# Optimization experiments

Hardware: AMD Instinct MI355X
Metric: run time of the kernel (lower is better)

The kernel has to match this reference:

```python
import jax, jax.numpy as jnp
import numpy as np

RES = 64
NU = 0.002
DX = 2.0 * np.pi / RES
DT = 0.001
M1 = 12
M2 = 12
WIDTH = 32


def _central(x, axis, dx):
    # periodic central difference via roll (matches torch.roll semantics)
    return (jnp.roll(x, -1, axis) - jnp.roll(x, 1, axis)) / (2.0 * dx)


def _grad_module(u):
    # TurbulenceRCLN.compute_grad_u: central diff in x,y; j==2 branch is u*0.1 (kept faithfully)
    g0 = _central(u, 2, DX)
    g1 = _central(u, 3, DX)
    g2 = u * 0.1
    return jnp.stack([g0, g1, g2], axis=2)  # (B,3,3,N,N,N) indexed [b,i,j]


def _grad_solver(u):
    # NavierStokesSolver._compute_gradient: true central differences in all 3 dirs
    return jnp.stack([_central(u, 2 + j, DX) for j in range(3)], axis=2)


def _laplacian(u):
    lap = jnp.zeros_like(u)
    for ax in (2, 3, 4):
        lap = lap + (jnp.roll(u, -1, ax) - 2.0 * u + jnp.roll(u, 1, ax)) / (DX * DX)
    return lap


def _div_tau(tau):
    # tau: (B,3,3,N,N,N); div_i = sum_j d tau_ij / dx_j
    return sum(_central(tau[:, :, j], 2 + j, DX) for j in range(3))


def _spectral_conv(x, w1, w2):
    # x: (B,C,N,N); w1/w2: (C,C,M1,M2,2) real/imag
    N = x.shape[-1]
    xft = jnp.fft.rfft2(x)  # (B,C,N,N//2+1) complex
    w1c = w1[..., 0] + 1j * w1[..., 1]
    w2c = w2[..., 0] + 1j * w2[..., 1]
    a = jnp.einsum('bixy,ioxy->boxy', xft[:, :, :M1, :M2], w1c)
    b = jnp.einsum('bixy,ioxy->boxy', xft[:, :, -M1:, :M2], w2c)
    out = jnp.zeros_like(xft).at[:, :, :M1, :M2].set(a).at[:, :, -M1:, :M2].set(b)
    return jnp.fft.irfft2(out, s=(N, N))


def _fno2d(x, fc0_w, fc0_b, spec_w1, spec_w2, conv_w, conv_b, fc1_w, fc1_b, fc2_w, fc2_b):
    h = jnp.einsum('bcxy,cd->bdxy', x, fc0_w) + fc0_b[None, :, None, None]
    for l in range(4):
        s = _spectral_conv(h, spec_w1[l], spec_w2[l])
        w = jnp.einsum('bcxy,co->boxy', h, conv_w[l]) + conv_b[l][None, :, None, None]
        h = s + w
        if l < 3:
            h = jax.nn.gelu(h)
    h = jax.nn.gelu(jnp.einsum('bcxy,cd->bdxy', h, fc1_w) + fc1_b[None, :, None, None])
    return jnp.einsum('bcxy,cd->bdxy', h, fc2_w) + fc2_b[None, :, None, None]


def setup_inputs() -> dict:
    key = jax.random.key(0)
    ks = jax.random.split(key, 8)
    B = 16
    scale = 1.0 / (WIDTH * WIDTH)
    return {
        'velocity': jax.random.normal(ks[0], (B, 3, RES, RES, RES), jnp.float32),
        'fc0_w': jax.random.normal(ks[1], (10, WIDTH), jnp.float32) * 0.1,
        'fc0_b': jnp.zeros((WIDTH,), jnp.float32),
        'spec_w1': jax.random.normal(ks[2], (4, WIDTH, WIDTH, M1, M2, 2), jnp.float32) * scale,
        'spec_w2': jax.random.normal(ks[3], (4, WIDTH, WIDTH, M1, M2, 2), jnp.float32) * scale,
        'conv_w': jax.random.normal(ks[4], (4, WIDTH, WIDTH), jnp.float32) * 0.1,
        'conv_b': jnp.zeros((4, WIDTH), jnp.float32),
        'fc1_w': jax.random.normal(ks[5], (WIDTH, 128), jnp.float32) * 0.1,
        'fc1_b': jnp.zeros((128,), jnp.float32),
        'fc2_w': jax.random.normal(ks[6], (128, 6), jnp.float32) * 0.1,
        'fc2_b': jnp.zeros((6,), jnp.float32),
    }


def reference(velocity, fc0_w, fc0_b, spec_w1, spec_w2, conv_w, conv_b, fc1_w, fc1_b, fc2_w, fc2_b):
    B = velocity.shape[0]
    N = RES
    # --- soft-shell closure input ---
    grad_u = _grad_module(velocity)                                   # (B,3,3,N,N,N)
    S = 0.5 * (grad_u + jnp.swapaxes(grad_u, 1, 2))
    S_mag = jnp.sqrt(2.0 * jnp.sum(S * S, axis=(1, 2), keepdims=True))  # (B,1,1,N,N,N)
    g_slice = grad_u[:, :, :, :, N // 2, :].reshape(B, 9, N, N)        # 9 grad channels at mid-plane
    s_slice = S_mag[:, :, :, :, N // 2, :].reshape(B, 1, N, N)         # 1 strain-mag channel
    closure_in = jnp.concatenate([g_slice, s_slice], axis=1)          # (B,10,N,N)
    tau2d = _fno2d(closure_in, fc0_w, fc0_b, spec_w1, spec_w2, conv_w, conv_b,
                   fc1_w, fc1_b, fc2_w, fc2_b)                         # (B,6,N,N)
    t = jnp.broadcast_to(tau2d[..., None], (B, 6, N, N, N))           # expand along z
    # reconstruct symmetric stress tensor (B,3,3,N,N,N)
    row0 = jnp.stack([t[:, 0], t[:, 3], t[:, 4]], axis=1)
    row1 = jnp.stack([t[:, 3], t[:, 1], t[:, 5]], axis=1)
    row2 = jnp.stack([t[:, 4], t[:, 5], t[:, 2]], axis=1)
    tau_full = jnp.stack([row0, row1, row2], axis=1)
    # --- hard-core NS step ---
    g = _grad_solver(velocity)
    lap = _laplacian(velocity)
    convection = jnp.einsum('bixyz,bijxyz->bjxyz', velocity, g)
    div_tau = _div_tau(tau_full)
    return velocity + DT * (-convection + NU * lap + div_tau)
```

## Files before the change

kernel.cpp:

```cpp
#include <hip/hip_runtime.h>
#include <math.h>

#define NRES 64
#define NXY  4096
#define NVOL 262144
#define BB   16
#define WID  32
#define MM   12
#define R24  24

constexpr double DX_d   = 2.0 * 3.14159265358979323846 / 64.0;
constexpr float  INV2DX = (float)(1.0 / (2.0 * DX_d));
constexpr float  INVDX2 = (float)(1.0 / (DX_d * DX_d));
constexpr float  DT_c   = 0.001f;
constexpr float  NU_c   = 0.002f;

constexpr size_t OFF_FR  = 0;
constexpr size_t OFF_FI  = OFF_FR + (size_t)R24 * NRES;
constexpr size_t OFF_GR  = OFF_FI + (size_t)R24 * NRES;
constexpr size_t OFF_GI  = OFF_GR + (size_t)MM * NRES;
constexpr size_t OFF_CL  = OFF_GI + (size_t)MM * NRES;
constexpr size_t OFF_HA  = OFF_CL + (size_t)BB * 10 * NXY;
constexpr size_t OFF_HB  = OFF_HA + (size_t)BB * WID * NXY;
constexpr size_t OFF_T1R = OFF_HB + (size_t)BB * WID * NXY;
constexpr size_t OFF_T1I = OFF_T1R + (size_t)BB * WID * R24 * NRES;
constexpr size_t OFF_XR  = OFF_T1I + (size_t)BB * WID * R24 * NRES;
constexpr size_t OFF_XI  = OFF_XR + (size_t)BB * WID * R24 * MM;
constexpr size_t OFF_MR  = OFF_XI + (size_t)BB * WID * R24 * MM;
constexpr size_t OFF_MI  = OFF_MR + (size_t)BB * WID * R24 * MM;
constexpr size_t OFF_AR  = OFF_MI + (size_t)BB * WID * R24 * MM;
constexpr size_t OFF_AI  = OFF_AR + (size_t)BB * WID * MM * NRES;
constexpr size_t OFF_H1  = OFF_AI + (size_t)BB * WID * MM * NRES;
constexpr size_t OFF_TAU = OFF_H1 + (size_t)BB * 128 * NXY;
constexpr size_t OFF_FRT = OFF_TAU + (size_t)BB * 6 * NXY;
constexpr size_t OFF_FIT = OFF_FRT + (size_t)NRES * R24;

constexpr size_t OFF_SP  = OFF_H1;
constexpr size_t OFF_W1T = OFF_H1 + (size_t)BB * WID * NXY;
constexpr size_t OFF_CWT = OFF_W1T + 4096;
constexpr size_t OFF_W0T = OFF_CWT + 4096;
constexpr size_t OFF_PT  = OFF_T1R;
constexpr size_t PT_STRIDE = (size_t)BB * 6 * NXY;

__device__ __forceinline__ float gelu_fast(float x) {
    float z = 0.79788456080286535588f * (x + 0.044715f * x * x * x);
    float e = __expf(2.0f * z);
    float t = 1.0f - 2.0f / (e + 1.0f);
    return 0.5f * x * (1.0f + t);
}

__device__ __forceinline__ float2 gelu2(float2 v) {
    return make_float2(gelu_fast(v.x), gelu_fast(v.y));
}

__global__ void k_setup(const float* __restrict__ fc1w, const float* __restrict__ convw,
                        const float* __restrict__ fc0w, float* __restrict__ ws) {
    int idx = blockIdx.x * 256 + threadIdx.x;
    if (idx < R24 * NRES) {
        int r = idx / NRES, x = idx % NRES;
        int kx = (r < MM) ? r : (r + 40);
        double ang = -2.0 * 3.14159265358979323846 * (double)(kx * x) / 64.0;
        float cr = (float)cos(ang), ci = (float)sin(ang);
        ws[OFF_FR + idx] = cr;
        ws[OFF_FI + idx] = ci;
        ws[OFF_FRT + (size_t)x * R24 + r] = cr;
        ws[OFF_FIT + (size_t)x * R24 + r] = ci;
    }
    if (idx < MM * NRES) {
        int ky = idx / NRES, y = idx % NRES;
        double ang = -2.0 * 3.14159265358979323846 * (double)(ky * y) / 64.0;
        ws[OFF_GR + idx] = (float)cos(ang);
        ws[OFF_GI + idx] = (float)sin(ang);
    }
    if (idx < 4096) {
        int c = idx >> 7, e = idx & 127;
        ws[OFF_W1T + (size_t)e * 32 + c] = fc1w[idx];
    } else if (idx < 8192) {
        int j = idx - 4096;
        int l = j >> 10, r = j & 1023;
        int c = r >> 5, o = r & 31;
        ws[OFF_CWT + (size_t)l * 1024 + o * 32 + c] = convw[j];
    } else if (idx < 8512) {
        int j = idx - 8192;
        int c = j >> 5, d = j & 31;
        ws[OFF_W0T + (size_t)d * 10 + c] = fc0w[j];
    }
}

__global__ void k_clfc0(const float* __restrict__ v, const float* __restrict__ w0t,
                        const float* __restrict__ bias, float* __restrict__ h) {
    __shared__ __align__(16) float sw[32 * 12];
    __shared__ float sb[32];
    int tid = threadIdx.x;
    for (int i = tid; i < 320; i += 256) {
        int d = i / 10, c = i % 10;
        sw[d * 12 + c] = w0t[i];
    }
    if (tid < 32) sb[tid] = bias[tid];
    __syncthreads();
    int idx = blockIdx.x * 256 + tid;
    int b = idx >> 10;
    int rr = idx & 1023;
    int x = rr >> 4, z0 = (rr & 15) * 4;
    int xp = (x + 1) & 63, xm = (x - 1) & 63;
    float4 cv[10];
    for (int i = 0; i < 3; i++) {
        const float* vb = v + (((size_t)(b * 3 + i)) << 18);
        float4 u4   = *(const float4*)(vb + (size_t)x  * 4096 + 32 * 64 + z0);
        float4 uxp4 = *(const float4*)(vb + (size_t)xp * 4096 + 32 * 64 + z0);
        float4 uxm4 = *(const float4*)(vb + (size_t)xm * 4096 + 32 * 64 + z0);
        float4 uyp4 = *(const float4*)(vb + (size_t)x  * 4096 + 33 * 64 + z0);
        float4 uym4 = *(const float4*)(vb + (size_t)x  * 4096 + 31 * 64 + z0);
        cv[i * 3 + 0] = make_float4((uxp4.x - uxm4.x) * INV2DX, (uxp4.y - uxm4.y) * INV2DX,
                                    (uxp4.z - uxm4.z) * INV2DX, (uxp4.w - uxm4.w) * INV2DX);
        cv[i * 3 + 1] = make_float4((uyp4.x - uym4.x) * INV2DX, (uyp4.y - uym4.y) * INV2DX,
                                    (uyp4.z - uym4.z) * INV2DX, (uyp4.w - uym4.w) * INV2DX);
        cv[i * 3 + 2] = make_float4(0.1f * u4.x, 0.1f * u4.y, 0.1f * u4.z, 0.1f * u4.w);
    }
    float4 ss = make_float4(0.f, 0.f, 0.f, 0.f);
    for (int i = 0; i < 3; i++)
        for (int j = 0; j < 3; j++) {
            float4 a = cv[i * 3 + j], bt = cv[j * 3 + i];
            float sx = 0.5f * (a.x + bt.x), sy = 0.5f * (a.y + bt.y);
            float sz = 0.5f * (a.z + bt.z), sw_ = 0.5f * (a.w + bt.w);
            ss.x += sx * sx; ss.y += sy * sy; ss.z += sz * sz; ss.w += sw_ * sw_;
        }
    cv[9] = make_float4(sqrtf(2.f * ss.x), sqrtf(2.f * ss.y),
                        sqrtf(2.f * ss.z), sqrtf(2.f * ss.w));
    float* hp = h + (size_t)b * WID * NXY + (size_t)x * 64 + z0;
#pragma unroll
    for (int d = 0; d < 32; d++) {
        float4 acc = make_float4(sb[d], sb[d], sb[d], sb[d]);
#pragma unroll
        for (int c = 0; c < 10; c++) {
            float w = sw[d * 12 + c];
            acc.x += w * cv[c].x; acc.y += w * cv[c].y;
            acc.z += w * cv[c].z; acc.w += w * cv[c].w;
        }
        *(float4*)(hp + (size_t)d * NXY) = acc;
    }
}

__global__ void k_fwd(const float* __restrict__ h, const float* __restrict__ ws,
                      float* __restrict__ xr, float* __restrict__ xi) {
    __shared__ __align__(16) float sh[4096];
    __shared__ float st1r[12 * 65];
    __shared__ float st1i[12 * 65];
    int tid = threadIdx.x;
    int blk = blockIdx.x;
    int bc = blk >> 1, half = blk & 1;
    int rbase = half * 12;
    const float4* hp4 = (const float4*)(h + (size_t)bc * NXY);
    float4* sh4 = (float4*)sh;
#pragma unroll
    for (int i = 0; i < 4; i++) sh4[tid + 256 * i] = hp4[tid + 256 * i];
    __syncthreads();
    const float* FRT = ws + OFF_FRT;
    const float* FIT = ws + OFF_FIT;
#pragma unroll
    for (int it = 0; it < 3; it++) {
        int point = it * 256 + tid;
        int y = point & 63;
        int rl = __builtin_amdgcn_readfirstlane(point >> 6);
        int rg = rbase + rl;
        float ar = 0.f, ai = 0.f;
#pragma unroll 16
        for (int x = 0; x < 64; x++) {
            float hv = sh[x * 64 + y];
            ar += hv * FRT[x * R24 + rg];
            ai += hv * FIT[x * R24 + rg];
        }
        st1r[rl * 65 + y] = ar;
        st1i[rl * 65 + y] = ai;
    }
    __syncthreads();
    const float* GR = ws + OFF_GR;
    const float* GI = ws + OFF_GI;
    if (tid < 144) {
        int rl = tid / 12, ky = tid - rl * 12;
        const float* Gr = GR + (size_t)ky * 64;
        const float* Gi = GI + (size_t)ky * 64;
        float ar = 0.f, ai = 0.f;
#pragma unroll 16
        for (int yy = 0; yy < 64; yy++) {
            float a = st1r[rl * 65 + yy], b = st1i[rl * 65 + yy];
            float c = Gr[yy], d = Gi[yy];
            ar += a * c - b * d;
            ai += a * d + b * c;
        }
        size_t outp = (size_t)bc * 288 + (size_t)(rbase + rl) * 12 + ky;
        xr[outp] = ar;
        xi[outp] = ai;
    }
}

__global__ void k_specinv(const float* __restrict__ xr, const float* __restrict__ xi,
                          const float* __restrict__ w1, const float* __restrict__ w2,
                          const float* __restrict__ ws, float* __restrict__ sp) {
    __shared__ float sm_r[288];
    __shared__ float sm_i[288];
    __shared__ float sa_r[12 * 64];
    __shared__ float sa_i[12 * 64];
    int tid = threadIdx.x;
    int bo = blockIdx.x;
    int o = bo & 31, b = bo >> 5;
    for (int m = tid; m < 288; m += 256) {
        int r = m / 12;
        int kxy = (r < MM) ? m : (m - 144);
        const float* wp = ((r < MM) ? w1 : w2) + ((size_t)o * 144 + kxy) * 2;
        size_t xbase = (size_t)b * 32 * 288 + m;
        float ar = 0.f, ai = 0.f;
#pragma unroll 8
        for (int i = 0; i < 32; i++) {
            float a   = xr[xbase + (size_t)i * 288];
            float bb  = xi[xbase + (size_t)i * 288];
            float wr_ = wp[(size_t)i * 9216];
            float wi_ = wp[(size_t)i * 9216 + 1];
            ar += a * wr_ - bb * wi_;
            ai += a * wi_ + bb * wr_;
        }
        sm_r[m] = ar; sm_i[m] = ai;
    }
    __syncthreads();
    const float* FR = ws + OFF_FR;
    const float* FI = ws + OFF_FI;
#pragma unroll
    for (int it = 0; it < 3; it++) {
        int point = it * 256 + tid;
        int x = point & 63;
        int ky = __builtin_amdgcn_readfirstlane(point >> 6);
        float ar = 0.f, ai = 0.f;
#pragma unroll 8
        for (int r = 0; r < 24; r++) {
            float a = sm_r[r * 12 + ky], bb = sm_i[r * 12 + ky];
            float c = FR[r * 64 + x], d = FI[r * 64 + x];
            ar += a * c + bb * d;
            ai += bb * c - a * d;
        }
        sa_r[ky * 64 + x] = ar;
        sa_i[ky * 64 + x] = ai;
    }
    __syncthreads();
    const float* GR = ws + OFF_GR;
    const float* GI = ws + OFF_GI;
    float* spb = sp + (size_t)bo * NXY;
#pragma unroll
    for (int it = 0; it < 16; it++) {
        int px = it * 256 + tid;
        int y = px & 63;
        int x = __builtin_amdgcn_readfirstlane(px >> 6);
        float s = sa_r[x];
#pragma unroll
        for (int ky = 1; ky < 12; ky++) {
            float gr = GR[ky * 64 + y];
            float gi = GI[ky * 64 + y];
            s += 2.0f * (sa_r[ky * 64 + x] * gr + sa_i[ky * 64 + x] * gi);
        }
        spb[px] = s * (1.0f / 4096.0f);
    }
}

template <int DOGELU>
__global__ void __launch_bounds__(256, 2)
k_convg(const float* __restrict__ sp, const float* __restrict__ hin,
        const float* __restrict__ cwt, const float* __restrict__ cb,
        float* __restrict__ hout) {
    __shared__ __align__(16) float scw[1024];
    __shared__ float scb[32];
    int tid = threadIdx.x;
#pragma unroll
    for (int i = 0; i < 4; i++) scw[tid + 256 * i] = cwt[tid + 256 * i];
    if (tid < 32) scb[tid] = cb[tid];
    __syncthreads();
    int wid = tid >> 6, lane = tid & 63;
    int blk = blockIdx.x;
    int osec = blk & 1;
    int q = (blk >> 1) * 64 + lane;
    int b = q >> 11, p = (q & 2047) * 2;
    const float* hp = hin + (size_t)b * WID * NXY + p;
    float2 hv[32];
#pragma unroll
    for (int c = 0; c < 32; c++) hv[c] = *(const float2*)(hp + (size_t)c * NXY);
    const float* spp = sp + (size_t)b * WID * NXY + p;
    float* op = hout + (size_t)b * WID * NXY + p;
#pragma unroll
    for (int j = 0; j < 4; j++) {
        int o = osec * 16 + wid * 4 + j;
        const float4* wr = (const float4*)&scw[o * 32];
        float2 d = make_float2(scb[o], scb[o]);
#pragma unroll
        for (int q8 = 0; q8 < 8; q8++) {
            float4 w = wr[q8];
            float2 h0 = hv[q8 * 4], h1 = hv[q8 * 4 + 1], h2 = hv[q8 * 4 + 2], h3 = hv[q8 * 4 + 3];
            d.x += w.x * h0.x + w.y * h1.x + w.z * h2.x + w.w * h3.x;
            d.y += w.x * h0.y + w.y * h1.y + w.z * h2.y + w.w * h3.y;
        }
        float2 spv = *(const float2*)(spp + (size_t)o * NXY);
        float2 v2 = make_float2(d.x + spv.x, d.y + spv.y);
        if (DOGELU) v2 = gelu2(v2);
        *(float2*)(op + (size_t)o * NXY) = v2;
    }
}

__global__ void __launch_bounds__(256, 2)
k_head(const float* __restrict__ h, const float* __restrict__ w1t,
       const float* __restrict__ b1, const float* __restrict__ w2,
       float* __restrict__ pt) {
    __shared__ __align__(16) float sw1[64 * 32];
    __shared__ float sb1l[64];
    __shared__ __align__(16) float sw2l[64 * 8];
    __shared__ __align__(8) float2 red[4][6][64];
    int tid = threadIdx.x;
    int blk = blockIdx.x;
    int esec = blk & 1;
    int ebase = esec * 64;
#pragma unroll
    for (int i = 0; i < 8; i++) sw1[tid + 256 * i] = w1t[(size_t)ebase * 32 + tid + 256 * i];
    if (tid < 64) sb1l[tid] = b1[ebase + tid];
    for (int i = tid; i < 384; i += 256) {
        int e = i / 6, t = i - e * 6;
        sw2l[e * 8 + t] = w2[(size_t)(ebase + e) * 6 + t];
    }
    __syncthreads();
    int wid = tid >> 6, lane = tid & 63;
    int q = (blk >> 1) * 64 + lane;
    int b = q >> 11, p = (q & 2047) * 2;
    const float* hp = h + (size_t)b * WID * NXY + p;
    float2 hv[32];
#pragma unroll
    for (int c = 0; c < 32; c++) hv[c] = *(const float2*)(hp + (size_t)c * NXY);
    float2 acc[6];
#pragma unroll
    for (int t = 0; t < 6; t++) acc[t] = make_float2(0.f, 0.f);
#pragma unroll 4
    for (int jj = 0; jj < 16; jj++) {
        int el = wid * 16 + jj;
        const float4* wr = (const float4*)&sw1[el * 32];
        float2 d = make_float2(sb1l[el], sb1l[el]);
#pragma unroll
        for (int q8 = 0; q8 < 8; q8++) {
            float4 w = wr[q8];
            float2 h0 = hv[q8 * 4], h1 = hv[q8 * 4 + 1], h2 = hv[q8 * 4 + 2], h3 = hv[q8 * 4 + 3];
            d.x += w.x * h0.x + w.y * h1.x + w.z * h2.x + w.w * h3.x;
            d.y += w.x * h0.y + w.y * h1.y + w.z * h2.y + w.w * h3.y;
        }
        float2 g = gelu2(d);
        const float4* w2r = (const float4*)&sw2l[el * 8];
        float4 wa = w2r[0], wb = w2r[1];
        acc[0].x += g.x * wa.x; acc[0].y += g.y * wa.x;
        acc[1].x += g.x * wa.y; acc[1].y += g.y * wa.y;
        acc[2].x += g.x * wa.z; acc[2].y += g.y * wa.z;
        acc[3].x += g.x * wa.w; acc[3].y += g.y * wa.w;
        acc[4].x += g.x * wb.x; acc[4].y += g.y * wb.x;
        acc[5].x += g.x * wb.y; acc[5].y += g.y * wb.y;
    }
#pragma unroll
    for (int t = 0; t < 6; t++) red[wid][t][lane] = acc[t];
    __syncthreads();
    if (wid == 0) {
        float* pb = pt + (size_t)esec * PT_STRIDE + (size_t)b * 6 * NXY + p;
#pragma unroll
        for (int t = 0; t < 6; t++) {
            float2 r0 = red[0][t][lane], r1 = red[1][t][lane];
            float2 r2 = red[2][t][lane], r3 = red[3][t][lane];
            float2 s = make_float2(r0.x + r1.x + r2.x + r3.x,
                                   r0.y + r1.y + r2.y + r3.y);
            *(float2*)(pb + (size_t)t * NXY) = s;
        }
    }
}

__global__ void k_tred(const float* __restrict__ pt, const float* __restrict__ b2,
                       float* __restrict__ tau) {
    int idx = blockIdx.x * 256 + threadIdx.x;
    int t = (idx >> 12) % 6;
    tau[idx] = pt[idx] + pt[idx + PT_STRIDE] + b2[t];
}

__global__ void __launch_bounds__(256, 2)
k_ns(const float* __restrict__ v, const float* __restrict__ tau,
     float* __restrict__ out) {
    int idx = blockIdx.x * 256 + threadIdx.x;
    int b = idx >> 16;
    int r = idx & 65535;
    int x = r >> 10;
    int y = (r >> 4) & 63;
    int z0 = (r & 15) * 4;
    int xp = (x + 1) & 63, xm = (x - 1) & 63;
    int yp = (y + 1) & 63, ym = (y - 1) & 63;
    int zm = (z0 - 1) & 63, zp = (z0 + 4) & 63;

    float4 u[3], gx[3], gy[3], gz[3], lap[3];
    for (int i = 0; i < 3; i++) {
        const float* vb = v + (((size_t)(b * 3 + i)) << 18);
        const float* row = vb + (size_t)x * 4096 + (size_t)y * 64;
        float4 c4   = *(const float4*)(row + z0);
        float  czm  = row[zm];
        float  czp  = row[zp];
        float4 xp4  = *(const float4*)(vb + (size_t)xp * 4096 + (size_t)y * 64 + z0);
        float4 xm4  = *(const float4*)(vb + (size_t)xm * 4096 + (size_t)y * 64 + z0);
        float4 yp4  = *(const float4*)(vb + (size_t)x * 4096 + (size_t)yp * 64 + z0);
        float4 ym4  = *(const float4*)(vb + (size_t)x * 4096 + (size_t)ym * 64 + z0);
        u[i] = c4;
        gx[i] = make_float4((xp4.x - xm4.x) * INV2DX, (xp4.y - xm4.y) * INV2DX,
                            (xp4.z - xm4.z) * INV2DX, (xp4.w - xm4.w) * INV2DX);
        gy[i] = make_float4((yp4.x - ym4.x) * INV2DX, (yp4.y - ym4.y) * INV2DX,
                            (yp4.z - ym4.z) * INV2DX, (yp4.w - ym4.w) * INV2DX);
        gz[i] = make_float4((c4.y - czm) * INV2DX, (c4.z - c4.x) * INV2DX,
                            (c4.w - c4.y) * INV2DX, (czp - c4.z) * INV2DX);
        lap[i] = make_float4(
            (xp4.x + xm4.x + yp4.x + ym4.x + czm  + c4.y - 6.f * c4.x) * INVDX2,
            (xp4.y + xm4.y + yp4.y + ym4.y + c4.x + c4.z - 6.f * c4.y) * INVDX2,
            (xp4.z + xm4.z + yp4.z + ym4.z + c4.y + c4.w - 6.f * c4.z) * INVDX2,
            (xp4.w + xm4.w + yp4.w + ym4.w + c4.z + czp  - 6.f * c4.w) * INVDX2);
    }
    const float* tb = tau + (size_t)b * 6 * NXY;
    int pxp = xp * 64 + y, pxm = xm * 64 + y, pyp = x * 64 + yp, pym = x * 64 + ym;
    float d0 = (tb[0 * NXY + pxp] - tb[0 * NXY + pxm]) * INV2DX +
               (tb[3 * NXY + pyp] - tb[3 * NXY + pym]) * INV2DX;
    float d1 = (tb[3 * NXY + pxp] - tb[3 * NXY + pxm]) * INV2DX +
               (tb[1 * NXY + pyp] - tb[1 * NXY + pym]) * INV2DX;
    float d2 = (tb[4 * NXY + pxp] - tb[4 * NXY + pxm]) * INV2DX +
               (tb[5 * NXY + pyp] - tb[5 * NXY + pym]) * INV2DX;

    size_t so = ((size_t)b * 3) * NVOL + (size_t)x * 4096 + (size_t)y * 64 + z0;
#pragma unroll
    for (int i = 0; i < 3; i++) {
        float dti = (i == 0) ? d0 : (i == 1) ? d1 : d2;
        float4 conv = make_float4(
            u[0].x * ((i==0)?gx[0].x:(i==1)?gy[0].x:gz[0].x) + u[1].x * ((i==0)?gx[1].x:(i==1)?gy[1].x:gz[1].x) + u[2].x * ((i==0)?gx[2].x:(i==1)?gy[2].x:gz[2].x),
            u[0].y * ((i==0)?gx[0].y:(i==1)?gy[0].y:gz[0].y) + u[1].y * ((i==0)?gx[1].y:(i==1)?gy[1].y:gz[1].y) + u[2].y * ((i==0)?gx[2].y:(i==1)?gy[2].y:gz[2].y),
            u[0].z * ((i==0)?gx[0].z:(i==1)?gy[0].z:gz[0].z) + u[1].z * ((i==0)?gx[1].z:(i==1)?gy[1].z:gz[1].z) + u[2].z * ((i==0)?gx[2].z:(i==1)?gy[2].z:gz[2].z),
            u[0].w * ((i==0)?gx[0].w:(i==1)?gy[0].w:gz[0].w) + u[1].w * ((i==0)?gx[1].w:(i==1)?gy[1].w:gz[1].w) + u[2].w * ((i==0)?gx[2].w:(i==1)?gy[2].w:gz[2].w));
        float4 res = make_float4(
            u[i].x + DT_c * (-conv.x + NU_c * lap[i].x + dti),
            u[i].y + DT_c * (-conv.y + NU_c * lap[i].y + dti),
            u[i].z + DT_c * (-conv.z + NU_c * lap[i].z + dti),
            u[i].w + DT_c * (-conv.w + NU_c * lap[i].w + dti));
        *(float4*)(out + so + (size_t)i * NVOL) = res;
    }
}

extern "C" void kernel_launch(void* const* d_in, const int* in_sizes, int n_in,
                              void* d_out, int out_size, void* d_ws, size_t ws_size,
                              hipStream_t stream) {
    const float* vel   = (const float*)d_in[0];
    const float* fc0w  = (const float*)d_in[1];
    const float* fc0b  = (const float*)d_in[2];
    const float* sw1   = (const float*)d_in[3];
    const float* sw2   = (const float*)d_in[4];
    const float* convw = (const float*)d_in[5];
    const float* convb = (const float*)d_in[6];
    const float* fc1w  = (const float*)d_in[7];
    const float* fc1b  = (const float*)d_in[8];
    const float* fc2w  = (const float*)d_in[9];
    const float* fc2b  = (const float*)d_in[10];
    float* ws  = (float*)d_ws;
    float* out = (float*)d_out;

    k_setup<<<34, 256, 0, stream>>>(fc1w, convw, fc0w, ws);
    k_clfc0<<<64, 256, 0, stream>>>(vel, ws + OFF_W0T, fc0b, ws + OFF_HA);

    float* hcur  = ws + OFF_HA;
    float* hnext = ws + OFF_HB;
    for (int l = 0; l < 4; l++) {
        const float* wl1 = sw1 + (size_t)l * WID * WID * MM * MM * 2;
        const float* wl2 = sw2 + (size_t)l * WID * WID * MM * MM * 2;
        const float* cwl = ws + OFF_CWT + (size_t)l * WID * WID;
        const float* cbl = convb + (size_t)l * WID;
        k_fwd<<<1024, 256, 0, stream>>>(hcur, ws, ws + OFF_XR, ws + OFF_XI);
        k_specinv<<<512, 256, 0, stream>>>(ws + OFF_XR, ws + OFF_XI, wl1, wl2, ws, ws + OFF_SP);
        if (l < 3)
            k_convg<1><<<1024, 256, 0, stream>>>(ws + OFF_SP, hcur, cwl, cbl, hnext);
        else
            k_convg<0><<<1024, 256, 0, stream>>>(ws + OFF_SP, hcur, cwl, cbl, hnext);
        float* tmp = hcur; hcur = hnext; hnext = tmp;
    }

    k_head<<<1024, 256, 0, stream>>>(hcur, ws + OFF_W1T, fc1b, fc2w, ws + OFF_PT);
    k_tred<<<1536, 256, 0, stream>>>(ws + OFF_PT, fc2b, ws + OFF_TAU);
    k_ns<<<4096, 256, 0, stream>>>(vel, ws + OFF_TAU, out);
}
```

Before: 238.5 us.

## Fuse spectral inverse with 1x1 conv+GELU and fold tau reduction into NS

The inverse spectral transform and the pointwise channel-mixing conv plus GELU now run in one kernel per (batch, output channel). The spectral result stays in shared memory instead of making a global round trip. The separate tau-reduction kernel is removed: the NS kernel sums the two partial head outputs directly and drops the fc2 bias, which cancels in the central differences. This saves launches and intermediate traffic, but each block now rereads all 32 input channels of h for its batch, which greatly increases L2 read traffic.

```diff
diff --git a/kernel.cpp b/kernel.cpp
--- a/kernel.cpp
+++ b/kernel.cpp
@@ -35,7 +35,6 @@
 constexpr size_t OFF_FRT = OFF_TAU + (size_t)BB * 6 * NXY;
 constexpr size_t OFF_FIT = OFF_FRT + (size_t)NRES * R24;
 
-constexpr size_t OFF_SP  = OFF_H1;
 constexpr size_t OFF_W1T = OFF_H1 + (size_t)BB * WID * NXY;
 constexpr size_t OFF_CWT = OFF_W1T + 4096;
 constexpr size_t OFF_W0T = OFF_CWT + 4096;
@@ -194,13 +193,18 @@
     }
 }
 
-__global__ void k_specinv(const float* __restrict__ xr, const float* __restrict__ xi,
-                          const float* __restrict__ w1, const float* __restrict__ w2,
-                          const float* __restrict__ ws, float* __restrict__ sp) {
+template <int DOGELU>
+__global__ void __launch_bounds__(256, 2)
+k_spc(const float* __restrict__ xr, const float* __restrict__ xi,
+      const float* __restrict__ w1, const float* __restrict__ w2,
+      const float* __restrict__ cwl, const float* __restrict__ cbl,
+      const float* __restrict__ ws, const float* __restrict__ hcur,
+      float* __restrict__ hnext) {
     __shared__ float sm_r[288];
     __shared__ float sm_i[288];
     __shared__ float sa_r[12 * 64];
     __shared__ float sa_i[12 * 64];
+    __shared__ __align__(16) float sp_l[4096];
     int tid = threadIdx.x;
     int bo = blockIdx.x;
     int o = bo & 31, b = bo >> 5;
@@ -243,62 +247,59 @@
     __syncthreads();
     const float* GR = ws + OFF_GR;
     const float* GI = ws + OFF_GI;
-    float* spb = sp + (size_t)bo * NXY;
-#pragma unroll
-    for (int it = 0; it < 16; it++) {
-        int px = it * 256 + tid;
-        int y = px & 63;
-        int x = __builtin_amdgcn_readfirstlane(px >> 6);
-        float s = sa_r[x];
+    {
+        int x = tid >> 2, ys = (tid & 3) * 16;
+        float a0 = sa_r[x];
+        float arv[11], aiv[11];
 #pragma unroll
         for (int ky = 1; ky < 12; ky++) {
-            float gr = GR[ky * 64 + y];
-            float gi = GI[ky * 64 + y];
-            s += 2.0f * (sa_r[ky * 64 + x] * gr + sa_i[ky * 64 + x] * gi);
-        }
-        spb[px] = s * (1.0f / 4096.0f);
-    }
-}
-
-template <int DOGELU>
-__global__ void __launch_bounds__(256, 2)
-k_convg(const float* __restrict__ sp, const float* __restrict__ hin,
-        const float* __restrict__ cwt, const float* __restrict__ cb,
-        float* __restrict__ hout) {
-    __shared__ __align__(16) float scw[1024];
-    __shared__ float scb[32];
-    int tid = threadIdx.x;
-#pragma unroll
-    for (int i = 0; i < 4; i++) scw[tid + 256 * i] = cwt[tid + 256 * i];
-    if (tid < 32) scb[tid] = cb[tid];
-    __syncthreads();
-    int wid = tid >> 6, lane = tid & 63;
-    int blk = blockIdx.x;
-    int osec = blk & 1;
-    int q = (blk >> 1) * 64 + lane;
-    int b = q >> 11, p = (q & 2047) * 2;
-    const float* hp = hin + (size_t)b * WID * NXY + p;
-    float2 hv[32];
-#pragma unroll
-    for (int c = 0; c < 32; c++) hv[c] = *(const float2*)(hp + (size_t)c * NXY);
-    const float* spp = sp + (size_t)b * WID * NXY + p;
-    float* op = hout + (size_t)b * WID * NXY + p;
-#pragma unroll
-    for (int j = 0; j < 4; j++) {
-        int o = osec * 16 + wid * 4 + j;
-        const float4* wr = (const float4*)&scw[o * 32];
-        float2 d = make_float2(scb[o], scb[o]);
-#pragma unroll
-        for (int q8 = 0; q8 < 8; q8++) {
-            float4 w = wr[q8];
-            float2 h0 = hv[q8 * 4], h1 = hv[q8 * 4 + 1], h2 = hv[q8 * 4 + 2], h3 = hv[q8 * 4 + 3];
-            d.x += w.x * h0.x + w.y * h1.x + w.z * h2.x + w.w * h3.x;
-            d.y += w.x * h0.y + w.y * h1.y + w.z * h2.y + w.w * h3.y;
-        }
-        float2 spv = *(const float2*)(spp + (size_t)o * NXY);
-        float2 v2 = make_float2(d.x + spv.x, d.y + spv.y);
-        if (DOGELU) v2 = gelu2(v2);
-        *(float2*)(op + (size_t)o * NXY) = v2;
+            arv[ky - 1] = sa_r[ky * 64 + x];
+            aiv[ky - 1] = sa_i[ky * 64 + x];
+        }
+#pragma unroll
+        for (int j = 0; j < 4; j++) {
+            int y0 = ys + j * 4;
+            float4 s = make_float4(a0, a0, a0, a0);
+#pragma unroll
+            for (int ky = 1; ky < 12; ky++) {
+                float4 g4r = *(const float4*)(GR + ky * 64 + y0);
+                float4 g4i = *(const float4*)(GI + ky * 64 + y0);
+                float ar = arv[ky - 1], ai = aiv[ky - 1];
+                s.x += 2.0f * (ar * g4r.x + ai * g4i.x);
+                s.y += 2.0f * (ar * g4r.y + ai * g4i.y);
+                s.z += 2.0f * (ar * g4r.z + ai * g4i.z);
+                s.w += 2.0f * (ar * g4r.w + ai * g4i.w);
+            }
+            s.x *= (1.0f / 4096.0f); s.y *= (1.0f / 4096.0f);
+            s.z *= (1.0f / 4096.0f); s.w *= (1.0f / 4096.0f);
+            *(float4*)(&sp_l[x * 64 + y0]) = s;
+        }
+    }
+    __syncthreads();
+    {
+        const float* wr = cwl + (size_t)o * 32;
+        float w[32];
+#pragma unroll
+        for (int c = 0; c < 32; c++) w[c] = wr[c];
+        float cb0 = cbl[o];
+        const float* hb = hcur + (size_t)b * WID * NXY;
+        float* ob = hnext + ((size_t)b * WID + o) * NXY;
+#pragma unroll 2
+        for (int it = 0; it < 8; it++) {
+            int q = it * 256 + tid;
+            int p = q * 2;
+            float2 d = make_float2(cb0, cb0);
+#pragma unroll
+            for (int c = 0; c < 32; c++) {
+                float2 hvv = *(const float2*)(hb + (size_t)c * NXY + p);
+                d.x += w[c] * hvv.x;
+                d.y += w[c] * hvv.y;
+            }
+            float2 spv = *(const float2*)(&sp_l[p]);
+            float2 v2 = make_float2(d.x + spv.x, d.y + spv.y);
+            if (DOGELU) v2 = gelu2(v2);
+            *(float2*)(ob + p) = v2;
+        }
     }
 }
 
@@ -370,15 +371,8 @@
     }
 }
 
-__global__ void k_tred(const float* __restrict__ pt, const float* __restrict__ b2,
-                       float* __restrict__ tau) {
-    int idx = blockIdx.x * 256 + threadIdx.x;
-    int t = (idx >> 12) % 6;
-    tau[idx] = pt[idx] + pt[idx + PT_STRIDE] + b2[t];
-}
-
 __global__ void __launch_bounds__(256, 2)
-k_ns(const float* __restrict__ v, const float* __restrict__ tau,
+k_ns(const float* __restrict__ v, const float* __restrict__ pt,
      float* __restrict__ out) {
     int idx = blockIdx.x * 256 + threadIdx.x;
     int b = idx >> 16;
@@ -414,14 +408,14 @@
             (xp4.z + xm4.z + yp4.z + ym4.z + c4.y + c4.w - 6.f * c4.z) * INVDX2,
             (xp4.w + xm4.w + yp4.w + ym4.w + c4.z + czp  - 6.f * c4.w) * INVDX2);
     }
-    const float* tb = tau + (size_t)b * 6 * NXY;
+    const float* p0 = pt + (size_t)b * 6 * NXY;
+    const float* p1 = p0 + PT_STRIDE;
     int pxp = xp * 64 + y, pxm = xm * 64 + y, pyp = x * 64 + yp, pym = x * 64 + ym;
-    float d0 = (tb[0 * NXY + pxp] - tb[0 * NXY + pxm]) * INV2DX +
-               (tb[3 * NXY + pyp] - tb[3 * NXY + pym]) * INV2DX;
-    float d1 = (tb[3 * NXY + pxp] - tb[3 * NXY + pxm]) * INV2DX +
-               (tb[1 * NXY + pyp] - tb[1 * NXY + pym]) * INV2DX;
-    float d2 = (tb[4 * NXY + pxp] - tb[4 * NXY + pxm]) * INV2DX +
-               (tb[5 * NXY + pyp] - tb[5 * NXY + pym]) * INV2DX;
+#define TV(t, pos) (p0[(size_t)(t) * NXY + (pos)] + p1[(size_t)(t) * NXY + (pos)])
+    float d0 = (TV(0, pxp) - TV(0, pxm)) * INV2DX + (TV(3, pyp) - TV(3, pym)) * INV2DX;
+    float d1 = (TV(3, pxp) - TV(3, pxm)) * INV2DX + (TV(1, pyp) - TV(1, pym)) * INV2DX;
+    float d2 = (TV(4, pxp) - TV(4, pxm)) * INV2DX + (TV(5, pyp) - TV(5, pym)) * INV2DX;
+#undef TV
 
     size_t so = ((size_t)b * 3) * NVOL + (size_t)x * 4096 + (size_t)y * 64 + z0;
 #pragma unroll
@@ -454,7 +448,6 @@
     const float* fc1w  = (const float*)d_in[7];
     const float* fc1b  = (const float*)d_in[8];
     const float* fc2w  = (const float*)d_in[9];
-    const float* fc2b  = (const float*)d_in[10];
     float* ws  = (float*)d_ws;
     float* out = (float*)d_out;
 
@@ -466,18 +459,18 @@
     for (int l = 0; l < 4; l++) {
         const float* wl1 = sw1 + (size_t)l * WID * WID * MM * MM * 2;
         const float* wl2 = sw2 + (size_t)l * WID * WID * MM * MM * 2;
-        const float* cwl = ws + OFF_CWT + (size_t)l * WID * WID;
-        const float* cbl = convb + (size_t)l * WID;
+        const float* cwl = ws + OFF_CWT + (size_t)l * 1024;
+        const float* cbl = convb + (size_t)l * 32;
         k_fwd<<<1024, 256, 0, stream>>>(hcur, ws, ws + OFF_XR, ws + OFF_XI);
-        k_specinv<<<512, 256, 0, stream>>>(ws + OFF_XR, ws + OFF_XI, wl1, wl2, ws, ws + OFF_SP);
         if (l < 3)
-            k_convg<1><<<1024, 256, 0, stream>>>(ws + OFF_SP, hcur, cwl, cbl, hnext);
+            k_spc<1><<<512, 256, 0, stream>>>(ws + OFF_XR, ws + OFF_XI, wl1, wl2,
+                                              cwl, cbl, ws, hcur, hnext);
         else
-            k_convg<0><<<1024, 256, 0, stream>>>(ws + OFF_SP, hcur, cwl, cbl, hnext);
+            k_spc<0><<<512, 256, 0, stream>>>(ws + OFF_XR, ws + OFF_XI, wl1, wl2,
+                                              cwl, cbl, ws, hcur, hnext);
         float* tmp = hcur; hcur = hnext; hnext = tmp;
     }
 
     k_head<<<1024, 256, 0, stream>>>(hcur, ws + OFF_W1T, fc1b, fc2w, ws + OFF_PT);
-    k_tred<<<1536, 256, 0, stream>>>(ws + OFF_PT, fc2b, ws + OFF_TAU);
-    k_ns<<<4096, 256, 0, stream>>>(vel, ws + OFF_TAU, out);
-}
+    k_ns<<<4096, 256, 0, stream>>>(vel, ws + OFF_PT, out);
+}
```

Result: slower. 302.7 us (+26.9%).

## Split spectral inverse into two half-mode blocks with separate partial outputs

Applied to the files above, without the earlier changes.

The spectral inverse kernel is split so that each block handles one of the two kx mode halves (w1 or w2), which doubles the grid to 1024 blocks and raises the occupancy hint. Each half writes its own partial spatial field into a second workspace buffer. The conv+gelu kernel then sums both partials. The aim is more parallelism, since the first stage previously had threads idle. The cost is twice the inverse-DFT store traffic and an extra read per output in the conv kernel.

```diff
diff --git a/kernel.cpp b/kernel.cpp
--- a/kernel.cpp
+++ b/kernel.cpp
@@ -36,7 +36,9 @@
 constexpr size_t OFF_FIT = OFF_FRT + (size_t)NRES * R24;
 
 constexpr size_t OFF_SP  = OFF_H1;
-constexpr size_t OFF_W1T = OFF_H1 + (size_t)BB * WID * NXY;
+constexpr size_t SPHALF  = (size_t)BB * WID * NXY;
+constexpr size_t OFF_SP2 = OFF_SP + SPHALF;
+constexpr size_t OFF_W1T = OFF_SP2 + SPHALF;
 constexpr size_t OFF_CWT = OFF_W1T + 4096;
 constexpr size_t OFF_W0T = OFF_CWT + 4096;
 constexpr size_t OFF_PT  = OFF_T1R;
@@ -194,21 +196,23 @@
     }
 }
 
-__global__ void k_specinv(const float* __restrict__ xr, const float* __restrict__ xi,
-                          const float* __restrict__ w1, const float* __restrict__ w2,
-                          const float* __restrict__ ws, float* __restrict__ sp) {
-    __shared__ float sm_r[288];
-    __shared__ float sm_i[288];
+__global__ void __launch_bounds__(256, 4)
+k_spch(const float* __restrict__ xr, const float* __restrict__ xi,
+       const float* __restrict__ w1, const float* __restrict__ w2,
+       const float* __restrict__ ws, float* __restrict__ sp) {
+    __shared__ float sm_r[144];
+    __shared__ float sm_i[144];
     __shared__ float sa_r[12 * 64];
     __shared__ float sa_i[12 * 64];
     int tid = threadIdx.x;
-    int bo = blockIdx.x;
-    int o = bo & 31, b = bo >> 5;
-    for (int m = tid; m < 288; m += 256) {
-        int r = m / 12;
-        int kxy = (r < MM) ? m : (m - 144);
-        const float* wp = ((r < MM) ? w1 : w2) + ((size_t)o * 144 + kxy) * 2;
-        size_t xbase = (size_t)b * 32 * 288 + m;
+    int blk = blockIdx.x;
+    int half = blk & 1;
+    int o = (blk >> 1) & 31;
+    int b = blk >> 6;
+    const float* wl = half ? w2 : w1;
+    if (tid < 144) {
+        const float* wp = wl + ((size_t)o * 144 + tid) * 2;
+        size_t xbase = (size_t)b * 32 * 288 + half * 144 + tid;
         float ar = 0.f, ai = 0.f;
 #pragma unroll 8
         for (int i = 0; i < 32; i++) {
@@ -219,7 +223,7 @@
             ar += a * wr_ - bb * wi_;
             ai += a * wi_ + bb * wr_;
         }
-        sm_r[m] = ar; sm_i[m] = ai;
+        sm_r[tid] = ar; sm_i[tid] = ai;
     }
     __syncthreads();
     const float* FR = ws + OFF_FR;
@@ -230,10 +234,11 @@
         int x = point & 63;
         int ky = __builtin_amdgcn_readfirstlane(point >> 6);
         float ar = 0.f, ai = 0.f;
-#pragma unroll 8
-        for (int r = 0; r < 24; r++) {
-            float a = sm_r[r * 12 + ky], bb = sm_i[r * 12 + ky];
-            float c = FR[r * 64 + x], d = FI[r * 64 + x];
+#pragma unroll 4
+        for (int rl = 0; rl < 12; rl++) {
+            float a = sm_r[rl * 12 + ky], bb = sm_i[rl * 12 + ky];
+            int rg = half * 12 + rl;
+            float c = FR[rg * 64 + x], d = FI[rg * 64 + x];
             ar += a * c + bb * d;
             ai += bb * c - a * d;
         }
@@ -243,7 +248,7 @@
     __syncthreads();
     const float* GR = ws + OFF_GR;
     const float* GI = ws + OFF_GI;
-    float* spb = sp + (size_t)bo * NXY;
+    float* spb = sp + (size_t)half * SPHALF + ((size_t)b * 32 + o) * NXY;
 #pragma unroll
     for (int it = 0; it < 16; it++) {
         int px = it * 256 + tid;
@@ -295,8 +300,9 @@
             d.x += w.x * h0.x + w.y * h1.x + w.z * h2.x + w.w * h3.x;
             d.y += w.x * h0.y + w.y * h1.y + w.z * h2.y + w.w * h3.y;
         }
-        float2 spv = *(const float2*)(spp + (size_t)o * NXY);
-        float2 v2 = make_float2(d.x + spv.x, d.y + spv.y);
+        float2 s0 = *(const float2*)(spp + (size_t)o * NXY);
+        float2 s1 = *(const float2*)(spp + SPHALF + (size_t)o * NXY);
+        float2 v2 = make_float2(d.x + s0.x + s1.x, d.y + s0.y + s1.y);
         if (DOGELU) v2 = gelu2(v2);
         *(float2*)(op + (size_t)o * NXY) = v2;
     }
@@ -466,10 +472,10 @@
     for (int l = 0; l < 4; l++) {
         const float* wl1 = sw1 + (size_t)l * WID * WID * MM * MM * 2;
         const float* wl2 = sw2 + (size_t)l * WID * WID * MM * MM * 2;
-        const float* cwl = ws + OFF_CWT + (size_t)l * WID * WID;
-        const float* cbl = convb + (size_t)l * WID;
+        const float* cwl = ws + OFF_CWT + (size_t)l * 1024;
+        const float* cbl = convb + (size_t)l * 32;
         k_fwd<<<1024, 256, 0, stream>>>(hcur, ws, ws + OFF_XR, ws + OFF_XI);
-        k_specinv<<<512, 256, 0, stream>>>(ws + OFF_XR, ws + OFF_XI, wl1, wl2, ws, ws + OFF_SP);
+        k_spch<<<1024, 256, 0, stream>>>(ws + OFF_XR, ws + OFF_XI, wl1, wl2, ws, ws + OFF_SP);
         if (l < 3)
             k_convg<1><<<1024, 256, 0, stream>>>(ws + OFF_SP, hcur, cwl, cbl, hnext);
         else
```

Measured after the change: 264.3 us. 1.11x slower.
